# Kernel optimization log

Hardware: AMD Instinct MI355X
Metric: run time of the kernel (lower is better)

## Reference

```python
import jax, jax.numpy as jnp
import numpy as np

V, D, H, N, L = 400000, 300, 300, 346, 50


def _lstm_scan(x, Wih, Whh, b, reverse):
    # x: (L, N, din); torch gate order i, f, g, o
    Hh = Whh.shape[1]
    def step(carry, xt):
        h, c = carry
        g = xt @ Wih.T + h @ Whh.T + b
        i, f, gg, o = jnp.split(g, 4, axis=-1)
        c = jax.nn.sigmoid(f) * c + jax.nn.sigmoid(i) * jnp.tanh(gg)
        h = jax.nn.sigmoid(o) * jnp.tanh(c)
        return (h, c), h
    h0 = jnp.zeros((x.shape[1], Hh), x.dtype)
    (hT, _), outs = jax.lax.scan(step, (h0, h0), x, reverse=reverse)
    return hT, outs  # outs stacked in original time order


def _gate(h, W, U):
    # Faithful to torch gate_module: g_i broadcast over rows makes
    # g.repeat @ h_x == g_i * sum(h_x) and (1-g).repeat @ h_c_rep == (1-g_i)*m*h_c
    h_c = h[0]
    h_x = h[1:]
    m = h_x.shape[0]
    g = jax.nn.sigmoid(h_x @ W + h_c @ U)  # (m, 1)
    h_tuta = g * jnp.sum(h_x, axis=0) + (1.0 - g) * (m * h_c)
    return jnp.concatenate([h_c[None, :], h_tuta], axis=0)


def _gat(h, mask, W, a):
    # standard pyGAT GraphAttentionLayer (concat=True -> elu), alpha=0.01
    Wh = h @ W                              # (N, out)
    F = W.shape[1]
    e = jax.nn.leaky_relu((Wh @ a[:F]) + (Wh @ a[F:]).T, 0.01)  # (N, N)
    att = jax.nn.softmax(jnp.where(mask, e, -9e15), axis=1)
    return jax.nn.elu(att @ Wh)


def _forward(emb, Wih_l0f, Whh_l0f, b_l0f, Wih_l0b, Whh_l0b, b_l0b,
             Wih_l1f, Whh_l1f, b_l1f, Wih_l1b, Whh_l1b, b_l1b,
             W_gat, a_gat, gate_W, gate_U, FC1, FC2, Wlin, blin,
             tokens, adj):
    tok = tokens[0]                        # (N, L)
    x = jnp.swapaxes(emb[tok], 0, 1)       # (L, N, 300)
    hf0, of0 = _lstm_scan(x, Wih_l0f, Whh_l0f, b_l0f, False)
    hb0, ob0 = _lstm_scan(x, Wih_l0b, Whh_l0b, b_l0b, True)
    o0 = jnp.concatenate([of0, ob0], axis=-1)   # (L, N, 600)
    hf1, _ = _lstm_scan(o0, Wih_l1f, Whh_l1f, b_l1f, False)
    hb1, _ = _lstm_scan(o0, Wih_l1b, Whh_l1b, b_l1b, True)
    # h_n layout [l0f, l0b, l1f, l1b] -> per-node concat = 1200
    hs0 = jnp.concatenate([hf0, hb0, hf1, hb1], axis=-1)
    mask = adj > 0
    hs1 = _gat(jnp.concatenate([hs0, _gate(hs0, gate_W, gate_U)], axis=1), mask, W_gat, a_gat)
    hs2 = _gat(jnp.concatenate([hs1, _gate(hs1, gate_W, gate_U)], axis=1), mask, W_gat, a_gat)
    hc = jnp.broadcast_to(hs2[0], hs2.shape)          # repeat(346, 1)
    hc3 = jnp.tanh(jnp.concatenate([hc, hs2, hc * hs2, hc - hs2], axis=1) @ FC1)
    b_att = jnp.tanh(hc3 @ FC2)                       # (N, 1)
    ea = jnp.concatenate([jnp.mean(hs2, axis=0, keepdims=True), b_att.T @ hs2], axis=1)
    return jax.nn.softmax(ea @ Wlin.T + blin, axis=1)  # (1, 2)


def setup_inputs() -> dict:
    key = jax.random.key(0)
    ks = iter(jax.random.split(key, 40))
    def rn(shape, scale=0.05):
        return jax.random.normal(next(ks), shape, dtype=jnp.float32) * scale
    inp = {}
    inp["tokens"] = jax.random.randint(next(ks), (1, N, L), 0, V)
    inp["adj"] = jax.random.randint(next(ks), (N, N), 0, 2).astype(jnp.int32)
    inp["emb"] = rn((V, D), 1.0)
    for name, din in (("l0f", D), ("l0b", D), ("l1f", 2 * H), ("l1b", 2 * H)):
        inp[f"Wih_{name}"] = rn((4 * H, din))
        inp[f"Whh_{name}"] = rn((4 * H, H))
        inp[f"b_{name}"] = rn((4 * H,))
    inp["W_gat"] = rn((2400, 1200))
    inp["a_gat"] = rn((2400, 1))
    inp["gate_W"] = rn((1200, 1))
    inp["gate_U"] = rn((1200, 1))
    inp["FC1"] = rn((4800, 9600), 0.01)
    inp["FC2"] = rn((9600, 1), 0.01)
    inp["Wlin"] = rn((2, 2400))
    inp["blin"] = rn((2,))
    return inp


def reference(tokens, adj, emb, Wih_l0f, Whh_l0f, b_l0f, Wih_l0b, Whh_l0b, b_l0b,
              Wih_l1f, Whh_l1f, b_l1f, Wih_l1b, Whh_l1b, b_l1b,
              W_gat, a_gat, gate_W, gate_U, FC1, FC2, Wlin, blin):
    return _forward(emb, Wih_l0f, Whh_l0f, b_l0f, Wih_l0b, Whh_l0b, b_l0b,
                    Wih_l1f, Whh_l1f, b_l1f, Wih_l1b, Whh_l1b, b_l1b,
                    W_gat, a_gat, gate_W, gate_U, FC1, FC2, Wlin, blin,
                    tokens, adj)
```

## Files before the change

### kernel.cpp

```cpp
#include <hip/hip_runtime.h>
#include <hip/hip_bf16.h>
#include <math.h>

typedef __hip_bfloat16 bf16;
typedef __attribute__((ext_vector_type(8))) short bf16x8;
typedef __attribute__((ext_vector_type(4))) float f32x4;

constexpr int kN  = 346;
constexpr int kL  = 50;
constexpr int kD  = 300;
constexpr int kH  = 300;
constexpr int kG  = 1200;
constexpr int kNL = kN * kL;
constexpr int kNLp = 17408;
constexpr int kNp  = 384;
constexpr int kKp0 = 320;
constexpr int kKp1 = 608;
constexpr int kGp  = 1280;

__device__ inline float toF(float v) { return v; }
__device__ inline float toF(bf16 v) { return __bfloat162float(v); }
__device__ inline void storeC(float* p, float v) { *p = v; }
__device__ inline void storeC(bf16* p, float v) { *p = __float2bfloat16(v); }
__device__ inline float sigf(float x) { return 1.f / (1.f + expf(-x)); }

template <int EPI, typename CT>
__global__ __launch_bounds__(256) void gemm_mfma(
    const bf16* __restrict__ A, const bf16* __restrict__ B, CT* __restrict__ C,
    int M, int N, int K, int lda, int ldb, int ldc,
    long sAz, long sBz, long sCz,
    const bf16* __restrict__ P, long sPz, const float* __restrict__ bias, long sbz)
{
    const short* Ag = (const short*)A + (size_t)blockIdx.z * sAz;
    const short* Bg = (const short*)B + (size_t)blockIdx.z * sBz;
    CT* Cg = C + (size_t)blockIdx.z * sCz;
    const bf16* Pg = nullptr; const float* bg = nullptr;
    if constexpr (EPI == 1) { Pg = P + (size_t)blockIdx.z * sPz; bg = bias + (size_t)blockIdx.z * sbz; }

    __shared__ short As[128 * 40];
    __shared__ short Bs[128 * 40];
    int tid = threadIdx.x;
    int row0 = blockIdx.y * 128, col0 = blockIdx.x * 128;
    int wave = tid >> 6, lane = tid & 63;
    int wr = (wave >> 1) * 64, wc = (wave & 1) * 64;
    int lrow = lane & 15, lq = lane >> 4;

    f32x4 acc[4][4];
#pragma unroll
    for (int i = 0; i < 4; ++i)
#pragma unroll
        for (int j = 0; j < 4; ++j) acc[i][j] = (f32x4){0.f, 0.f, 0.f, 0.f};

    int sr = tid >> 2;
    int sc = (tid & 3) * 8;
    for (int k0 = 0; k0 < K; k0 += 32) {
        *(bf16x8*)&As[sr * 40 + sc]        = *(const bf16x8*)&Ag[(size_t)(row0 + sr) * lda + k0 + sc];
        *(bf16x8*)&As[(sr + 64) * 40 + sc] = *(const bf16x8*)&Ag[(size_t)(row0 + sr + 64) * lda + k0 + sc];
        *(bf16x8*)&Bs[sr * 40 + sc]        = *(const bf16x8*)&Bg[(size_t)(col0 + sr) * ldb + k0 + sc];
        *(bf16x8*)&Bs[(sr + 64) * 40 + sc] = *(const bf16x8*)&Bg[(size_t)(col0 + sr + 64) * ldb + k0 + sc];
        __syncthreads();
        bf16x8 aF[4], bF[4];
#pragma unroll
        for (int i = 0; i < 4; ++i) aF[i] = *(const bf16x8*)&As[(wr + i * 16 + lrow) * 40 + lq * 8];
#pragma unroll
        for (int j = 0; j < 4; ++j) bF[j] = *(const bf16x8*)&Bs[(wc + j * 16 + lrow) * 40 + lq * 8];
#pragma unroll
        for (int i = 0; i < 4; ++i)
#pragma unroll
            for (int j = 0; j < 4; ++j)
                acc[i][j] = __builtin_amdgcn_mfma_f32_16x16x32_bf16(aF[i], bF[j], acc[i][j], 0, 0, 0);
        __syncthreads();
    }
#pragma unroll
    for (int i = 0; i < 4; ++i) {
#pragma unroll
        for (int r = 0; r < 4; ++r) {
            int gm = row0 + wr + i * 16 + lq * 4 + r;
            if (gm >= M) continue;
#pragma unroll
            for (int j = 0; j < 4; ++j) {
                int gn = col0 + wc + j * 16 + lrow;
                if (gn >= N) continue;
                float v = acc[i][j][r];
                if constexpr (EPI == 1) v += toF(Pg[(size_t)gm * ldc + gn]) + bg[gn];
                if constexpr (EPI == 3) v = v > 0.f ? v : (expf(v) - 1.f);
                if constexpr (EPI == 4) v = tanhf(v);
                storeC(&Cg[(size_t)gm * ldc + gn], v);
            }
        }
    }
}

__global__ void transpose_conv(const float* __restrict__ in, bf16* __restrict__ out,
                               int R, int Cc, int Rpad, int Cpad) {
    __shared__ float tile[32][33];
    int bc = blockIdx.x * 32, br = blockIdx.y * 32;
    int tx = threadIdx.x & 31, ty = threadIdx.x >> 5;
#pragma unroll
    for (int k = 0; k < 4; ++k) {
        int r = br + ty + 8 * k, c = bc + tx;
        tile[ty + 8 * k][tx] = (r < R && c < Cc) ? in[(size_t)r * Cc + c] : 0.f;
    }
    __syncthreads();
#pragma unroll
    for (int k = 0; k < 4; ++k) {
        int c = bc + ty + 8 * k, r = br + tx;
        if (c < Cpad && r < Rpad) out[(size_t)c * Rpad + r] = __float2bfloat16(tile[tx][ty + 8 * k]);
    }
}

__global__ void convert_pad(const float* __restrict__ in, bf16* __restrict__ out,
                            int R, int Cc, int Rpad, int Cpad) {
    int idx = blockIdx.x * 256 + threadIdx.x;
    if (idx >= Rpad * Cpad) return;
    int r = idx / Cpad, c = idx - r * Cpad;
    float v = (r < R && c < Cc) ? in[(size_t)r * Cc + c] : 0.f;
    out[idx] = __float2bfloat16(v);
}

__global__ void pack_biases(const float* b0f, const float* b0b, const float* b1f,
                            const float* b1b, float* b0, float* b1) {
    int i = blockIdx.x * 256 + threadIdx.x;
    if (i < 1200) { b0[i] = b0f[i]; b1[i] = b1f[i]; }
    else if (i < 2400) { b0[i] = b0b[i - 1200]; b1[i] = b1b[i - 1200]; }
}

__global__ void gather_kernel(const int* __restrict__ tokens, const float* __restrict__ emb,
                              bf16* __restrict__ x) {
    int idx = blockIdx.x * 256 + threadIdx.x;
    if (idx >= kNLp * kKp0) return;
    int row = idx / kKp0, d = idx - row * kKp0;
    float v = 0.f;
    if (row < kNL && d < kD) {
        int l = row / kN, n = row - l * kN;
        v = emb[(size_t)tokens[n * kL + l] * kD + d];
    }
    x[idx] = __float2bfloat16(v);
}

__global__ void lstm_point(const float* __restrict__ g, float* __restrict__ c,
                           bf16* __restrict__ hbf, bf16* __restrict__ o0, int tf, int tb) {
    int idx = blockIdx.x * 256 + threadIdx.x;
    if (idx >= 2 * kN * kH) return;
    int dir = idx / (kN * kH);
    int rem = idx - dir * kN * kH;
    int r = rem / kH, j = rem - r * kH;
    const float* gr = g + (size_t)dir * kN * kG + (size_t)r * kG;
    float iv = sigf(gr[j]);
    float fv = sigf(gr[j + kH]);
    float gv = tanhf(gr[j + 2 * kH]);
    float ov = sigf(gr[j + 3 * kH]);
    float cc = fv * c[idx] + iv * gv;
    c[idx] = cc;
    float hh = ov * tanhf(cc);
    hbf[(size_t)dir * kNp * kKp0 + (size_t)r * kKp0 + j] = __float2bfloat16(hh);
    if (o0) {
        int t = dir ? tb : tf;
        o0[(size_t)(t * kN + r) * kKp1 + dir * kH + j] = __float2bfloat16(hh);
    }
}

__global__ void concat_hs0(const bf16* __restrict__ hbf0, const bf16* __restrict__ hbf1,
                           float* __restrict__ hs0) {
    int idx = blockIdx.x * 256 + threadIdx.x;
    if (idx >= kN * kG) return;
    int r = idx / kG, c = idx - r * kG;
    float v;
    if (c < 300)       v = toF(hbf0[(size_t)r * kKp0 + c]);
    else if (c < 600)  v = toF(hbf0[(size_t)(kNp + r) * kKp0 + (c - 300)]);
    else if (c < 900)  v = toF(hbf1[(size_t)r * kKp0 + (c - 600)]);
    else               v = toF(hbf1[(size_t)(kNp + r) * kKp0 + (c - 900)]);
    hs0[idx] = v;
}

__global__ void colsum_kernel(const float* __restrict__ hs, float* __restrict__ sum_hx) {
    int c = blockIdx.x * 256 + threadIdx.x;
    if (c >= kG) return;
    float s = 0.f;
    for (int r = 1; r < kN; ++r) s += hs[(size_t)r * kG + c];
    sum_hx[c] = s;
}

__global__ void gate_rows(const float* __restrict__ hs, const float* __restrict__ gW,
                          const float* __restrict__ gU, const float* __restrict__ sum_hx,
                          bf16* __restrict__ hin) {
    __shared__ float red[256];
    int n = blockIdx.x, tid = threadIdx.x;
    for (int c = tid; c < kG; c += 256)
        hin[(size_t)n * 2400 + c] = __float2bfloat16(hs[(size_t)n * kG + c]);
    if (n == 0) {
        for (int c = tid; c < kG; c += 256)
            hin[1200 + c] = __float2bfloat16(hs[c]);
        return;
    }
    float dw = 0.f, du = 0.f;
    for (int c = tid; c < kG; c += 256) {
        dw += hs[(size_t)n * kG + c] * gW[c];
        du += hs[c] * gU[c];
    }
    red[tid] = dw; __syncthreads();
    for (int s = 128; s > 0; s >>= 1) { if (tid < s) red[tid] += red[tid + s]; __syncthreads(); }
    float sdw = red[0]; __syncthreads();
    red[tid] = du; __syncthreads();
    for (int s = 128; s > 0; s >>= 1) { if (tid < s) red[tid] += red[tid + s]; __syncthreads(); }
    float sdu = red[0]; __syncthreads();
    float gval = sigf(sdw + sdu);
    for (int c = tid; c < kG; c += 256) {
        float v = gval * sum_hx[c] + (1.f - gval) * (345.f * hs[c]);
        hin[(size_t)n * 2400 + 1200 + c] = __float2bfloat16(v);
    }
}

__global__ void gat_scores(const float* __restrict__ Wh, const float* __restrict__ a,
                           float* __restrict__ s1, float* __restrict__ s2) {
    __shared__ float red[256];
    int n = blockIdx.x, tid = threadIdx.x;
    float d1 = 0.f, d2 = 0.f;
    for (int c = tid; c < kG; c += 256) {
        float w = Wh[(size_t)n * kG + c];
        d1 += w * a[c];
        d2 += w * a[kG + c];
    }
    red[tid] = d1; __syncthreads();
    for (int s = 128; s > 0; s >>= 1) { if (tid < s) red[tid] += red[tid + s]; __syncthreads(); }
    if (tid == 0) s1[n] = red[0];
    __syncthreads();
    red[tid] = d2; __syncthreads();
    for (int s = 128; s > 0; s >>= 1) { if (tid < s) red[tid] += red[tid + s]; __syncthreads(); }
    if (tid == 0) s2[n] = red[0];
}

__global__ void gat_softmax(const float* __restrict__ s1, const float* __restrict__ s2,
                            const int* __restrict__ adj, bf16* __restrict__ att) {
    __shared__ float red[256];
    __shared__ float sh_m, sh_s;
    int i = blockIdx.x, tid = threadIdx.x;
    float s1i = s1[i];
    float m = -1e30f;
    for (int j = tid; j < kN; j += 256) {
        if (adj[i * kN + j] > 0) {
            float e = s1i + s2[j];
            e = e > 0.f ? e : 0.01f * e;
            m = fmaxf(m, e);
        }
    }
    red[tid] = m; __syncthreads();
    for (int s = 128; s > 0; s >>= 1) { if (tid < s) red[tid] = fmaxf(red[tid], red[tid + s]); __syncthreads(); }
    if (tid == 0) sh_m = red[0];
    __syncthreads();
    m = sh_m;
    float sum = 0.f;
    for (int j = tid; j < kN; j += 256) {
        if (adj[i * kN + j] > 0) {
            float e = s1i + s2[j];
            e = e > 0.f ? e : 0.01f * e;
            sum += expf(e - m);
        }
    }
    red[tid] = sum; __syncthreads();
    for (int s = 128; s > 0; s >>= 1) { if (tid < s) red[tid] += red[tid + s]; __syncthreads(); }
    if (tid == 0) sh_s = red[0];
    __syncthreads();
    float inv = sh_s > 0.f ? 1.f / sh_s : 0.f;
    for (int j = tid; j < kN; j += 256) {
        float v = 0.f;
        if (adj[i * kN + j] > 0) {
            float e = s1i + s2[j];
            e = e > 0.f ? e : 0.01f * e;
            v = expf(e - m) * inv;
        }
        att[(size_t)i * 352 + j] = __float2bfloat16(v);
    }
}

__global__ void build_cat4(const float* __restrict__ hs2, bf16* __restrict__ cat4) {
    int idx = blockIdx.x * 256 + threadIdx.x;
    if (idx >= kN * 4800) return;
    int r = idx / 4800, c = idx - r * 4800;
    int chunk = c / kG, cc = c - chunk * kG;
    float hc = hs2[cc];
    float hv = hs2[(size_t)r * kG + cc];
    float v = (chunk == 0) ? hc : (chunk == 1) ? hv : (chunk == 2) ? hc * hv : (hc - hv);
    cat4[idx] = __float2bfloat16(v);
}

__global__ void row_dot_tanh(const float* __restrict__ hc3, const float* __restrict__ FC2,
                             float* __restrict__ b_att) {
    __shared__ float red[256];
    int n = blockIdx.x, tid = threadIdx.x;
    float d = 0.f;
    for (int c = tid; c < 9600; c += 256) d += hc3[(size_t)n * 9600 + c] * FC2[c];
    red[tid] = d; __syncthreads();
    for (int s = 128; s > 0; s >>= 1) { if (tid < s) red[tid] += red[tid + s]; __syncthreads(); }
    if (tid == 0) b_att[n] = tanhf(red[0]);
}

__global__ void ea_kernel(const float* __restrict__ hs2, const float* __restrict__ b_att,
                          float* __restrict__ ea) {
    int c = blockIdx.x * 256 + threadIdx.x;
    if (c >= kG) return;
    float s = 0.f, w = 0.f;
    for (int r = 0; r < kN; ++r) {
        float v = hs2[(size_t)r * kG + c];
        s += v;
        w += b_att[r] * v;
    }
    ea[c] = s / (float)kN;
    ea[kG + c] = w;
}

__global__ void final_kernel(const float* __restrict__ ea, const float* __restrict__ Wlin,
                             const float* __restrict__ blin, float* __restrict__ out) {
    __shared__ float red[256];
    int tid = threadIdx.x;
    float l0 = 0.f, l1 = 0.f;
    for (int c = tid; c < 2400; c += 256) {
        float e = ea[c];
        l0 += e * Wlin[c];
        l1 += e * Wlin[2400 + c];
    }
    red[tid] = l0; __syncthreads();
    for (int s = 128; s > 0; s >>= 1) { if (tid < s) red[tid] += red[tid + s]; __syncthreads(); }
    l0 = red[0]; __syncthreads();
    red[tid] = l1; __syncthreads();
    for (int s = 128; s > 0; s >>= 1) { if (tid < s) red[tid] += red[tid + s]; __syncthreads(); }
    l1 = red[0];
    if (tid == 0) {
        l0 += blin[0];
        l1 += blin[1];
        float m = fmaxf(l0, l1);
        float e0 = expf(l0 - m), e1 = expf(l1 - m);
        float inv = 1.f / (e0 + e1);
        out[0] = e0 * inv;
        out[1] = e1 * inv;
    }
}

extern "C" void kernel_launch(void* const* d_in, const int* in_sizes, int n_in,
                              void* d_out, int out_size, void* d_ws, size_t ws_size,
                              hipStream_t stream) {
    const int*   tokens  = (const int*)d_in[0];
    const int*   adj     = (const int*)d_in[1];
    const float* emb     = (const float*)d_in[2];
    const float* Wih_l0f = (const float*)d_in[3];
    const float* Whh_l0f = (const float*)d_in[4];
    const float* b_l0f   = (const float*)d_in[5];
    const float* Wih_l0b = (const float*)d_in[6];
    const float* Whh_l0b = (const float*)d_in[7];
    const float* b_l0b   = (const float*)d_in[8];
    const float* Wih_l1f = (const float*)d_in[9];
    const float* Whh_l1f = (const float*)d_in[10];
    const float* b_l1f   = (const float*)d_in[11];
    const float* Wih_l1b = (const float*)d_in[12];
    const float* Whh_l1b = (const float*)d_in[13];
    const float* b_l1b   = (const float*)d_in[14];
    const float* W_gat   = (const float*)d_in[15];
    const float* a_gat   = (const float*)d_in[16];
    const float* gate_W  = (const float*)d_in[17];
    const float* gate_U  = (const float*)d_in[18];
    const float* FC1     = (const float*)d_in[19];
    const float* FC2     = (const float*)d_in[20];
    const float* Wlin    = (const float*)d_in[21];
    const float* blin    = (const float*)d_in[22];
    float* out = (float*)d_out;
    (void)in_sizes; (void)n_in; (void)out_size; (void)ws_size;

    char* base = (char*)d_ws;
    size_t off = 0;
    auto alloc = [&](size_t bytes) {
        size_t cur = off;
        off += (bytes + 255) & ~(size_t)255;
        return base + cur;
    };

    const size_t xPad_sz = (size_t)kNLp * kKp0 * 2;
    const size_t P_sz    = (size_t)2 * kNL * kG * 2;
    char* regA = alloc(94181120);
    bf16* xPad  = (bf16*)(regA);
    bf16* P0    = (bf16*)(regA + xPad_sz);
    bf16* P1    = (bf16*)(regA);
    bf16* WgatT = (bf16*)(regA);
    bf16* hin   = (bf16*)(regA + 6144000);
    bf16* att   = (bf16*)(regA + 7987200);
    bf16* FC1T  = (bf16*)(regA);
    const size_t gatScratch_sz = 8257536;
    (void)P_sz;

    char* o0r   = alloc((size_t)kNLp * kKp1 * 2);
    bf16*  o0   = (bf16*)o0r;
    float* hc3  = (float*)o0r;

    float* g    = (float*)alloc((size_t)2 * kN * kG * 4);
    char* stateblk = alloc(2 * 830400 + 2 * 491520);
    float* c0   = (float*)(stateblk);
    float* c1   = (float*)(stateblk + 830400);
    bf16*  hbf0 = (bf16*)(stateblk + 2 * 830400);
    bf16*  hbf1 = (bf16*)(stateblk + 2 * 830400 + 491520);
    const size_t state_sz = 2 * 830400 + 2 * 491520;

    bf16* Wih0 = (bf16*)alloc((size_t)2 * kGp * kKp0 * 2);
    bf16* Wih1 = (bf16*)alloc((size_t)2 * kGp * kKp1 * 2);
    bf16* Whh0 = (bf16*)alloc((size_t)2 * kGp * kKp0 * 2);
    bf16* Whh1 = (bf16*)alloc((size_t)2 * kGp * kKp0 * 2);
    float* b0p = (float*)alloc(2400 * 4);
    float* b1p = (float*)alloc(2400 * 4);
    float* hsA = (float*)alloc((size_t)kN * kG * 4);
    float* hsB = (float*)alloc((size_t)kN * kG * 4);
    float* sum_hx = (float*)alloc(kG * 4);
    float* Wh  = (float*)alloc((size_t)kN * kG * 4);
    bf16*  WhT = (bf16*)alloc((size_t)kGp * 352 * 2);
    float* s1  = (float*)alloc(kN * 4);
    float* s2  = (float*)alloc(kN * 4);
    bf16*  cat4 = (bf16*)alloc((size_t)kNp * 4800 * 2);
    float* b_att = (float*)alloc(kN * 4);
    float* ea  = (float*)alloc(2400 * 4);

    hipMemsetAsync(stateblk, 0, state_sz, stream);
    hipMemsetAsync(o0r, 0, (size_t)kNLp * kKp1 * 2, stream);
    hipMemsetAsync(cat4, 0, (size_t)kNp * 4800 * 2, stream);

    pack_biases<<<10, 256, 0, stream>>>(b_l0f, b_l0b, b_l1f, b_l1b, b0p, b1p);
    int cpb0 = (kGp * kKp0 + 255) / 256;
    int cpb1 = (kGp * kKp1 + 255) / 256;
    convert_pad<<<cpb0, 256, 0, stream>>>(Wih_l0f, Wih0,              kG, kD,     kGp, kKp0);
    convert_pad<<<cpb0, 256, 0, stream>>>(Wih_l0b, Wih0 + kGp * kKp0, kG, kD,     kGp, kKp0);
    convert_pad<<<cpb1, 256, 0, stream>>>(Wih_l1f, Wih1,              kG, 2 * kH, kGp, kKp1);
    convert_pad<<<cpb1, 256, 0, stream>>>(Wih_l1b, Wih1 + kGp * kKp1, kG, 2 * kH, kGp, kKp1);
    convert_pad<<<cpb0, 256, 0, stream>>>(Whh_l0f, Whh0,              kG, kH,     kGp, kKp0);
    convert_pad<<<cpb0, 256, 0, stream>>>(Whh_l0b, Whh0 + kGp * kKp0, kG, kH,     kGp, kKp0);
    convert_pad<<<cpb0, 256, 0, stream>>>(Whh_l1f, Whh1,              kG, kH,     kGp, kKp0);
    convert_pad<<<cpb0, 256, 0, stream>>>(Whh_l1b, Whh1 + kGp * kKp0, kG, kH,     kGp, kKp0);

    gather_kernel<<<(kNLp * kKp0 + 255) / 256, 256, 0, stream>>>(tokens, emb, xPad);

    gemm_mfma<0, bf16><<<dim3(10, kNLp / 128, 2), 256, 0, stream>>>(
        xPad, Wih0, P0, kNL, kG, kKp0, kKp0, kKp0, kG,
        0, (long)kGp * kKp0, (long)kNL * kG, nullptr, 0, nullptr, 0);

    const long sC = (long)kN * kG;
    int ptBlocks = (2 * kN * kH + 255) / 256;
    for (int t = 0; t < kL; ++t) {
        long sP = (long)kNL * kG + (long)(kL - 1 - 2 * t) * kN * kG;
        gemm_mfma<1, float><<<dim3(10, 3, 2), 256, 0, stream>>>(
            hbf0, Whh0, g, kN, kG, kKp0, kKp0, kKp0, kG,
            (long)kNp * kKp0, (long)kGp * kKp0, sC,
            P0 + (size_t)t * kN * kG, sP, b0p, 1200);
        lstm_point<<<ptBlocks, 256, 0, stream>>>(g, c0, hbf0, o0, t, kL - 1 - t);
    }

    gemm_mfma<0, bf16><<<dim3(10, kNLp / 128, 2), 256, 0, stream>>>(
        o0, Wih1, P1, kNL, kG, kKp1, kKp1, kKp1, kG,
        0, (long)kGp * kKp1, (long)kNL * kG, nullptr, 0, nullptr, 0);

    for (int t = 0; t < kL; ++t) {
        long sP = (long)kNL * kG + (long)(kL - 1 - 2 * t) * kN * kG;
        gemm_mfma<1, float><<<dim3(10, 3, 2), 256, 0, stream>>>(
            hbf1, Whh1, g, kN, kG, kKp0, kKp0, kKp0, kG,
            (long)kNp * kKp0, (long)kGp * kKp0, sC,
            P1 + (size_t)t * kN * kG, sP, b1p, 1200);
        lstm_point<<<ptBlocks, 256, 0, stream>>>(g, c1, hbf1, (bf16*)nullptr, t, kL - 1 - t);
    }

    concat_hs0<<<(kN * kG + 255) / 256, 256, 0, stream>>>(hbf0, hbf1, hsA);

    hipMemsetAsync(regA, 0, gatScratch_sz, stream);
    transpose_conv<<<dim3(kGp / 32, 2400 / 32), 256, 0, stream>>>(W_gat, WgatT, 2400, kG, 2400, kGp);

    float* hsIn = hsA;
    float* hsOut = hsB;
    for (int it = 0; it < 2; ++it) {
        colsum_kernel<<<(kG + 255) / 256, 256, 0, stream>>>(hsIn, sum_hx);
        gate_rows<<<kN, 256, 0, stream>>>(hsIn, gate_W, gate_U, sum_hx, hin);
        gemm_mfma<0, float><<<dim3(10, 3, 1), 256, 0, stream>>>(
            hin, WgatT, Wh, kN, kG, 2400, 2400, 2400, kG,
            0, 0, 0, nullptr, 0, nullptr, 0);
        gat_scores<<<kN, 256, 0, stream>>>(Wh, a_gat, s1, s2);
        gat_softmax<<<kN, 256, 0, stream>>>(s1, s2, adj, att);
        transpose_conv<<<dim3(kGp / 32, 352 / 32), 256, 0, stream>>>(Wh, WhT, kN, kG, 352, kGp);
        gemm_mfma<3, float><<<dim3(10, 3, 1), 256, 0, stream>>>(
            att, WhT, hsOut, kN, kG, 352, 352, 352, kG,
            0, 0, 0, nullptr, 0, nullptr, 0);
        float* tmp = hsIn; hsIn = hsOut; hsOut = tmp;
    }

    build_cat4<<<(kN * 4800 + 255) / 256, 256, 0, stream>>>(hsIn, cat4);
    transpose_conv<<<dim3(9600 / 32, 4800 / 32), 256, 0, stream>>>(FC1, FC1T, 4800, 9600, 4800, 9600);
    gemm_mfma<4, float><<<dim3(75, 3, 1), 256, 0, stream>>>(
        cat4, FC1T, hc3, kN, 9600, 4800, 4800, 4800, 9600,
        0, 0, 0, nullptr, 0, nullptr, 0);
    row_dot_tanh<<<kN, 256, 0, stream>>>(hc3, FC2, b_att);
    ea_kernel<<<(kG + 255) / 256, 256, 0, stream>>>(hsIn, b_att, ea);
    final_kernel<<<1, 256, 0, stream>>>(ea, Wlin, blin, out);
}
```

Baseline: 4.388 ms.

## Fuse LSTM recurrence into persistent kernel with grid barriers and gate-interleaved weights

Replaces the 200 per-timestep launches (a recurrent GEMM plus a pointwise kernel per step, per layer) with one persistent kernel per layer. Each block keeps its Whh tile resident in LDS and keeps the cell state in registers. Gates are computed in the GEMM epilogue through an LDS transpose, and blocks sharing a row tile synchronise with an atomic group barrier each step. Weights and biases are permuted so the four gates of each hidden unit are adjacent, which makes the fusion possible. This removes launch overhead and the global round trips for the gates and cell state, at the cost of spin-wait barriers that depend on all 60 blocks being co-resident.

```diff
diff --git a/kernel.cpp b/kernel.cpp
--- a/kernel.cpp
+++ b/kernel.cpp
@@ -4,6 +4,7 @@
 
 typedef __hip_bfloat16 bf16;
 typedef __attribute__((ext_vector_type(8))) short bf16x8;
+typedef __attribute__((ext_vector_type(4))) short bf16x4;
 typedef __attribute__((ext_vector_type(4))) float f32x4;
 
 constexpr int kN  = 346;
@@ -17,12 +18,21 @@
 constexpr int kKp0 = 320;
 constexpr int kKp1 = 608;
 constexpr int kGp  = 1280;
+constexpr int kHB  = 384;
 
 __device__ inline float toF(float v) { return v; }
 __device__ inline float toF(bf16 v) { return __bfloat162float(v); }
 __device__ inline void storeC(float* p, float v) { *p = v; }
 __device__ inline void storeC(bf16* p, float v) { *p = __float2bfloat16(v); }
 __device__ inline float sigf(float x) { return 1.f / (1.f + expf(-x)); }
+__device__ inline float bfbits2f(unsigned short u) {
+    unsigned int x = ((unsigned int)u) << 16;
+    float f; __builtin_memcpy(&f, &x, 4); return f;
+}
+__device__ inline short f2bf_bits(float f) {
+    bf16 b = __float2bfloat16(f);
+    short s; __builtin_memcpy(&s, &b, 2); return s;
+}
 
 template <int EPI, typename CT>
 __global__ __launch_bounds__(256) void gemm_mfma(
@@ -34,8 +44,7 @@
     const short* Ag = (const short*)A + (size_t)blockIdx.z * sAz;
     const short* Bg = (const short*)B + (size_t)blockIdx.z * sBz;
     CT* Cg = C + (size_t)blockIdx.z * sCz;
-    const bf16* Pg = nullptr; const float* bg = nullptr;
-    if constexpr (EPI == 1) { Pg = P + (size_t)blockIdx.z * sPz; bg = bias + (size_t)blockIdx.z * sbz; }
+    (void)P; (void)sPz; (void)bias; (void)sbz;
 
     __shared__ short As[128 * 40];
     __shared__ short Bs[128 * 40];
@@ -82,7 +91,6 @@
                 int gn = col0 + wc + j * 16 + lrow;
                 if (gn >= N) continue;
                 float v = acc[i][j][r];
-                if constexpr (EPI == 1) v += toF(Pg[(size_t)gm * ldc + gn]) + bg[gn];
                 if constexpr (EPI == 3) v = v > 0.f ? v : (expf(v) - 1.f);
                 if constexpr (EPI == 4) v = tanhf(v);
                 storeC(&Cg[(size_t)gm * ldc + gn], v);
@@ -109,20 +117,28 @@
     }
 }
 
-__global__ void convert_pad(const float* __restrict__ in, bf16* __restrict__ out,
-                            int R, int Cc, int Rpad, int Cpad) {
+__global__ void convert_pad_perm(const float* __restrict__ in, bf16* __restrict__ out,
+                                 int Cc, int Cpad) {
     int idx = blockIdx.x * 256 + threadIdx.x;
-    if (idx >= Rpad * Cpad) return;
-    int r = idx / Cpad, c = idx - r * Cpad;
-    float v = (r < R && c < Cc) ? in[(size_t)r * Cc + c] : 0.f;
+    if (idx >= kGp * Cpad) return;
+    int rp = idx / Cpad, c = idx - rp * Cpad;
+    int j = rp >> 2, q = rp & 3;
+    float v = (j < kH && c < Cc) ? in[(size_t)(q * kH + j) * Cc + c] : 0.f;
     out[idx] = __float2bfloat16(v);
 }
 
-__global__ void pack_biases(const float* b0f, const float* b0b, const float* b1f,
-                            const float* b1b, float* b0, float* b1) {
+__global__ void pack_biases_perm(const float* b0f, const float* b0b, const float* b1f,
+                                 const float* b1b, float* b0, float* b1) {
     int i = blockIdx.x * 256 + threadIdx.x;
-    if (i < 1200) { b0[i] = b0f[i]; b1[i] = b1f[i]; }
-    else if (i < 2400) { b0[i] = b0b[i - 1200]; b1[i] = b1b[i - 1200]; }
+    if (i >= 2 * kGp) return;
+    int dir = i / kGp, rp = i - dir * kGp;
+    int j = rp >> 2, q = rp & 3;
+    float v0 = 0.f, v1 = 0.f;
+    if (j < kH) {
+        v0 = dir ? b0b[q * kH + j] : b0f[q * kH + j];
+        v1 = dir ? b1b[q * kH + j] : b1f[q * kH + j];
+    }
+    b0[i] = v0; b1[i] = v1;
 }
 
 __global__ void gather_kernel(const int* __restrict__ tokens, const float* __restrict__ emb,
@@ -138,25 +154,168 @@
     x[idx] = __float2bfloat16(v);
 }
 
-__global__ void lstm_point(const float* __restrict__ g, float* __restrict__ c,
-                           bf16* __restrict__ hbf, bf16* __restrict__ o0, int tf, int tb) {
-    int idx = blockIdx.x * 256 + threadIdx.x;
-    if (idx >= 2 * kN * kH) return;
-    int dir = idx / (kN * kH);
-    int rem = idx - dir * kN * kH;
-    int r = rem / kH, j = rem - r * kH;
-    const float* gr = g + (size_t)dir * kN * kG + (size_t)r * kG;
-    float iv = sigf(gr[j]);
-    float fv = sigf(gr[j + kH]);
-    float gv = tanhf(gr[j + 2 * kH]);
-    float ov = sigf(gr[j + 3 * kH]);
-    float cc = fv * c[idx] + iv * gv;
-    c[idx] = cc;
-    float hh = ov * tanhf(cc);
-    hbf[(size_t)dir * kNp * kKp0 + (size_t)r * kKp0 + j] = __float2bfloat16(hh);
-    if (o0) {
-        int t = dir ? tb : tf;
-        o0[(size_t)(t * kN + r) * kKp1 + dir * kH + j] = __float2bfloat16(hh);
+__device__ inline void group_barrier(int* bar, int target) {
+    __syncthreads();
+    if (threadIdx.x == 0) {
+        __threadfence();
+        __hip_atomic_fetch_add(bar, 1, __ATOMIC_RELAXED, __HIP_MEMORY_SCOPE_AGENT);
+        while (__hip_atomic_load(bar, __ATOMIC_RELAXED, __HIP_MEMORY_SCOPE_AGENT) < target)
+            __builtin_amdgcn_s_sleep(2);
+    }
+    __syncthreads();
+    __threadfence();
+}
+
+template <bool WRITE_O0>
+__global__ __launch_bounds__(256, 1) void lstm_scan_fused(
+    const bf16* __restrict__ WhhP,
+    const bf16* __restrict__ P,
+    const float* __restrict__ biasP,
+    bf16* __restrict__ hst,
+    bf16* __restrict__ o0,
+    int* __restrict__ bars)
+{
+    __shared__ short Bs[10][128][32];
+    __shared__ float Gs[4 * 32 * 128];
+
+    const int tid = threadIdx.x;
+    const int bx  = blockIdx.x;
+    const int cb  = bx % 10;
+    const int rb  = (bx / 10) % 3;
+    const int dir = bx / 30;
+    int* bar = bars + dir * 3 + rb;
+
+    const int wave = tid >> 6, lane = tid & 63;
+    const int wr = (wave >> 1) * 64, wc = (wave & 1) * 64;
+    const int lrow = lane & 15, lq = lane >> 4;
+    const int col0 = cb * 128, row0 = rb * 128;
+
+    {
+        const short* Bg = (const short*)WhhP + (size_t)dir * kGp * kKp0;
+        int sr = tid >> 2;
+        int g  = tid & 3;
+#pragma unroll
+        for (int ch = 0; ch < 10; ++ch) {
+            *(bf16x8*)&Bs[ch][sr][(g ^ ((sr >> 1) & 3)) * 8] =
+                *(const bf16x8*)&Bg[(size_t)(col0 + sr) * kKp0 + ch * 32 + g * 8];
+            *(bf16x8*)&Bs[ch][sr + 64][(g ^ (((sr + 64) >> 1) & 3)) * 8] =
+                *(const bf16x8*)&Bg[(size_t)(col0 + sr + 64) * kKp0 + ch * 32 + g * 8];
+        }
+    }
+
+    const int jj0 = (tid >> 5) * 4;
+    const int pr0 = (tid & 31) * 4;
+    const int jg0 = cb * 32 + jj0;
+    const bool jok = jg0 < kH;
+
+    float bias[4][4];
+#pragma unroll
+    for (int m = 0; m < 4; ++m) {
+        f32x4 b4 = *(const f32x4*)&biasP[dir * kGp + col0 + (jj0 + m) * 4];
+#pragma unroll
+        for (int q = 0; q < 4; ++q) bias[m][q] = b4[q];
+    }
+    float cst[4][4];
+#pragma unroll
+    for (int m = 0; m < 4; ++m)
+#pragma unroll
+        for (int r = 0; r < 4; ++r) cst[m][r] = 0.f;
+
+    short* o0s = (short*)o0;
+    __syncthreads();
+
+#pragma unroll 1
+    for (int t = 0; t < kL; ++t) {
+        const short* hr = (const short*)hst + ((size_t)(t & 1) * 2 + dir) * (kHB * kKp0);
+        short* hw = (short*)hst + ((size_t)((t + 1) & 1) * 2 + dir) * (kHB * kKp0);
+        const int teff = dir ? (kL - 1 - t) : t;
+        const short* Pt = (const short*)P + (size_t)dir * kNL * kG + (size_t)teff * kN * kG;
+
+        bf16x4 pv[4][4];
+        if (jok) {
+#pragma unroll
+            for (int m = 0; m < 4; ++m)
+#pragma unroll
+                for (int rr = 0; rr < 4; ++rr) {
+                    int rg = row0 + pr0 + rr;
+                    if (rg < kN)
+                        pv[m][rr] = *(const bf16x4*)&Pt[(size_t)rg * kG + (size_t)(jg0 + m) * 4];
+                }
+        }
+
+        f32x4 acc[4][4];
+#pragma unroll
+        for (int i = 0; i < 4; ++i)
+#pragma unroll
+            for (int j = 0; j < 4; ++j) acc[i][j] = (f32x4){0.f, 0.f, 0.f, 0.f};
+
+#pragma unroll
+        for (int ch = 0; ch < 10; ++ch) {
+            bf16x8 aF[4], bF[4];
+#pragma unroll
+            for (int i = 0; i < 4; ++i)
+                aF[i] = *(const bf16x8*)&hr[(size_t)(row0 + wr + i * 16 + lrow) * kKp0 + ch * 32 + lq * 8];
+#pragma unroll
+            for (int j = 0; j < 4; ++j) {
+                int brow = wc + j * 16 + lrow;
+                bF[j] = *(const bf16x8*)&Bs[ch][brow][(lq ^ ((brow >> 1) & 3)) * 8];
+            }
+#pragma unroll
+            for (int i = 0; i < 4; ++i)
+#pragma unroll
+                for (int j = 0; j < 4; ++j)
+                    acc[i][j] = __builtin_amdgcn_mfma_f32_16x16x32_bf16(aF[i], bF[j], acc[i][j], 0, 0, 0);
+        }
+
+#pragma unroll
+        for (int i = 0; i < 4; ++i) {
+            int r0 = wr + i * 16 + lq * 4;
+#pragma unroll
+            for (int j = 0; j < 4; ++j) {
+                int c = wc + j * 16 + lrow;
+                int q = c & 3, jj = c >> 2;
+                *(f32x4*)&Gs[(q * 32 + jj) * 128 + (r0 ^ ((jj & 7) << 2))] = acc[i][j];
+            }
+        }
+        __syncthreads();
+
+        if (jok) {
+            float hval[4][4];
+#pragma unroll
+            for (int m = 0; m < 4; ++m) {
+                int jjl = jj0 + m;
+                int sw = (jjl & 7) << 2;
+                f32x4 gi4 = *(const f32x4*)&Gs[(0 * 32 + jjl) * 128 + (pr0 ^ sw)];
+                f32x4 gf4 = *(const f32x4*)&Gs[(1 * 32 + jjl) * 128 + (pr0 ^ sw)];
+                f32x4 gg4 = *(const f32x4*)&Gs[(2 * 32 + jjl) * 128 + (pr0 ^ sw)];
+                f32x4 go4 = *(const f32x4*)&Gs[(3 * 32 + jjl) * 128 + (pr0 ^ sw)];
+#pragma unroll
+                for (int rr = 0; rr < 4; ++rr) {
+                    int rg = row0 + pr0 + rr;
+                    if (rg >= kN) continue;
+                    float iv = sigf(gi4[rr] + bfbits2f((unsigned short)pv[m][rr][0]) + bias[m][0]);
+                    float fv = sigf(gf4[rr] + bfbits2f((unsigned short)pv[m][rr][1]) + bias[m][1]);
+                    float gv = tanhf(gg4[rr] + bfbits2f((unsigned short)pv[m][rr][2]) + bias[m][2]);
+                    float ov = sigf(go4[rr] + bfbits2f((unsigned short)pv[m][rr][3]) + bias[m][3]);
+                    float cc = fv * cst[m][rr] + iv * gv;
+                    cst[m][rr] = cc;
+                    hval[rr][m] = ov * tanhf(cc);
+                }
+            }
+#pragma unroll
+            for (int rr = 0; rr < 4; ++rr) {
+                int rg = row0 + pr0 + rr;
+                if (rg >= kN) continue;
+                bf16x4 hv;
+#pragma unroll
+                for (int m = 0; m < 4; ++m) hv[m] = f2bf_bits(hval[rr][m]);
+                *(bf16x4*)&hw[(size_t)rg * kKp0 + jg0] = hv;
+                if constexpr (WRITE_O0)
+                    *(bf16x4*)&o0s[((size_t)teff * kN + rg) * kKp1 + dir * kH + jg0] = hv;
+            }
+        }
+
+        group_barrier(bar, 10 * (t + 1));
     }
 }
 
@@ -374,7 +533,6 @@
     };
 
     const size_t xPad_sz = (size_t)kNLp * kKp0 * 2;
-    const size_t P_sz    = (size_t)2 * kNL * kG * 2;
     char* regA = alloc(94181120);
     bf16* xPad  = (bf16*)(regA);
     bf16* P0    = (bf16*)(regA + xPad_sz);
@@ -384,26 +542,23 @@
     bf16* att   = (bf16*)(regA + 7987200);
     bf16* FC1T  = (bf16*)(regA);
     const size_t gatScratch_sz = 8257536;
-    (void)P_sz;
 
     char* o0r   = alloc((size_t)kNLp * kKp1 * 2);
     bf16*  o0   = (bf16*)o0r;
     float* hc3  = (float*)o0r;
 
-    float* g    = (float*)alloc((size_t)2 * kN * kG * 4);
-    char* stateblk = alloc(2 * 830400 + 2 * 491520);
-    float* c0   = (float*)(stateblk);
-    float* c1   = (float*)(stateblk + 830400);
-    bf16*  hbf0 = (bf16*)(stateblk + 2 * 830400);
-    bf16*  hbf1 = (bf16*)(stateblk + 2 * 830400 + 491520);
-    const size_t state_sz = 2 * 830400 + 2 * 491520;
+    const size_t hst_sz = (size_t)2 * 2 * kHB * kKp0 * 2;
+    char* hblk = alloc(hst_sz * 2 + 256);
+    bf16* hstA = (bf16*)hblk;
+    bf16* hstB = (bf16*)(hblk + hst_sz);
+    int*  bars = (int*)(hblk + 2 * hst_sz);
 
     bf16* Wih0 = (bf16*)alloc((size_t)2 * kGp * kKp0 * 2);
     bf16* Wih1 = (bf16*)alloc((size_t)2 * kGp * kKp1 * 2);
     bf16* Whh0 = (bf16*)alloc((size_t)2 * kGp * kKp0 * 2);
     bf16* Whh1 = (bf16*)alloc((size_t)2 * kGp * kKp0 * 2);
-    float* b0p = (float*)alloc(2400 * 4);
-    float* b1p = (float*)alloc(2400 * 4);
+    float* b0p = (float*)alloc(2 * kGp * 4);
+    float* b1p = (float*)alloc(2 * kGp * 4);
     float* hsA = (float*)alloc((size_t)kN * kG * 4);
     float* hsB = (float*)alloc((size_t)kN * kG * 4);
     float* sum_hx = (float*)alloc(kG * 4);
@@ -415,21 +570,21 @@
     float* b_att = (float*)alloc(kN * 4);
     float* ea  = (float*)alloc(2400 * 4);
 
-    hipMemsetAsync(stateblk, 0, state_sz, stream);
+    hipMemsetAsync(hblk, 0, hst_sz * 2 + 256, stream);
     hipMemsetAsync(o0r, 0, (size_t)kNLp * kKp1 * 2, stream);
     hipMemsetAsync(cat4, 0, (size_t)kNp * 4800 * 2, stream);
 
-    pack_biases<<<10, 256, 0, stream>>>(b_l0f, b_l0b, b_l1f, b_l1b, b0p, b1p);
-    int cpb0 = (kGp * kKp0 + 255) / 256;
-    int cpb1 = (kGp * kKp1 + 255) / 256;
-    convert_pad<<<cpb0, 256, 0, stream>>>(Wih_l0f, Wih0,              kG, kD,     kGp, kKp0);
-    convert_pad<<<cpb0, 256, 0, stream>>>(Wih_l0b, Wih0 + kGp * kKp0, kG, kD,     kGp, kKp0);
-    convert_pad<<<cpb1, 256, 0, stream>>>(Wih_l1f, Wih1,              kG, 2 * kH, kGp, kKp1);
-    convert_pad<<<cpb1, 256, 0, stream>>>(Wih_l1b, Wih1 + kGp * kKp1, kG, 2 * kH, kGp, kKp1);
-    convert_pad<<<cpb0, 256, 0, stream>>>(Whh_l0f, Whh0,              kG, kH,     kGp, kKp0);
-    convert_pad<<<cpb0, 256, 0, stream>>>(Whh_l0b, Whh0 + kGp * kKp0, kG, kH,     kGp, kKp0);
-    convert_pad<<<cpb0, 256, 0, stream>>>(Whh_l1f, Whh1,              kG, kH,     kGp, kKp0);
-    convert_pad<<<cpb0, 256, 0, stream>>>(Whh_l1b, Whh1 + kGp * kKp0, kG, kH,     kGp, kKp0);
+    pack_biases_perm<<<10, 256, 0, stream>>>(b_l0f, b_l0b, b_l1f, b_l1b, b0p, b1p);
+    int cpp0 = (kGp * kKp0 + 255) / 256;
+    int cpp1 = (kGp * kKp1 + 255) / 256;
+    convert_pad_perm<<<cpp0, 256, 0, stream>>>(Wih_l0f, Wih0,              kD,     kKp0);
+    convert_pad_perm<<<cpp0, 256, 0, stream>>>(Wih_l0b, Wih0 + kGp * kKp0, kD,     kKp0);
+    convert_pad_perm<<<cpp1, 256, 0, stream>>>(Wih_l1f, Wih1,              2 * kH, kKp1);
+    convert_pad_perm<<<cpp1, 256, 0, stream>>>(Wih_l1b, Wih1 + kGp * kKp1, 2 * kH, kKp1);
+    convert_pad_perm<<<cpp0, 256, 0, stream>>>(Whh_l0f, Whh0,              kH,     kKp0);
+    convert_pad_perm<<<cpp0, 256, 0, stream>>>(Whh_l0b, Whh0 + kGp * kKp0, kH,     kKp0);
+    convert_pad_perm<<<cpp0, 256, 0, stream>>>(Whh_l1f, Whh1,              kH,     kKp0);
+    convert_pad_perm<<<cpp0, 256, 0, stream>>>(Whh_l1b, Whh1 + kGp * kKp0, kH,     kKp0);
 
     gather_kernel<<<(kNLp * kKp0 + 255) / 256, 256, 0, stream>>>(tokens, emb, xPad);
 
@@ -437,31 +592,15 @@
         xPad, Wih0, P0, kNL, kG, kKp0, kKp0, kKp0, kG,
         0, (long)kGp * kKp0, (long)kNL * kG, nullptr, 0, nullptr, 0);
 
-    const long sC = (long)kN * kG;
-    int ptBlocks = (2 * kN * kH + 255) / 256;
-    for (int t = 0; t < kL; ++t) {
-        long sP = (long)kNL * kG + (long)(kL - 1 - 2 * t) * kN * kG;
-        gemm_mfma<1, float><<<dim3(10, 3, 2), 256, 0, stream>>>(
-            hbf0, Whh0, g, kN, kG, kKp0, kKp0, kKp0, kG,
-            (long)kNp * kKp0, (long)kGp * kKp0, sC,
-            P0 + (size_t)t * kN * kG, sP, b0p, 1200);
-        lstm_point<<<ptBlocks, 256, 0, stream>>>(g, c0, hbf0, o0, t, kL - 1 - t);
-    }
+    lstm_scan_fused<true><<<60, 256, 0, stream>>>(Whh0, P0, b0p, hstA, o0, bars);
 
     gemm_mfma<0, bf16><<<dim3(10, kNLp / 128, 2), 256, 0, stream>>>(
         o0, Wih1, P1, kNL, kG, kKp1, kKp1, kKp1, kG,
         0, (long)kGp * kKp1, (long)kNL * kG, nullptr, 0, nullptr, 0);
 
-    for (int t = 0; t < kL; ++t) {
-        long sP = (long)kNL * kG + (long)(kL - 1 - 2 * t) * kN * kG;
-        gemm_mfma<1, float><<<dim3(10, 3, 2), 256, 0, stream>>>(
-            hbf1, Whh1, g, kN, kG, kKp0, kKp0, kKp0, kG,
-            (long)kNp * kKp0, (long)kGp * kKp0, sC,
-            P1 + (size_t)t * kN * kG, sP, b1p, 1200);
-        lstm_point<<<ptBlocks, 256, 0, stream>>>(g, c1, hbf1, (bf16*)nullptr, t, kL - 1 - t);
-    }
-
-    concat_hs0<<<(kN * kG + 255) / 256, 256, 0, stream>>>(hbf0, hbf1, hsA);
+    lstm_scan_fused<false><<<60, 256, 0, stream>>>(Whh1, P1, b1p, hstB, nullptr, bars + 6);
+
+    concat_hs0<<<(kN * kG + 255) / 256, 256, 0, stream>>>(hstA, hstB, hsA);
 
     hipMemsetAsync(regA, 0, gatScratch_sz, stream);
     transpose_conv<<<dim3(kGp / 32, 2400 / 32), 256, 0, stream>>>(W_gat, WgatT, 2400, kG, 2400, kGp);
```

New measurement: 3.709 ms. -15.5%, faster.
